# Kernel tuning notes

Hardware: AMD Instinct MI355X
Metric: run time of the kernel (lower is better)

## Reference

```python
import jax, jax.numpy as jnp
import numpy as np

NUM_HEADS = 16


def setup_inputs() -> dict:
    key = jax.random.key(0)
    ks = jax.random.split(key, 8)
    B, W, D = 128, 512, 2048
    s = 1.0 / np.sqrt(D)
    return {
        "x": jax.random.normal(ks[0], (B, D), jnp.float32),
        "buffer": jax.random.normal(ks[1], (B, W, D), jnp.float32),
        "Wq": jax.random.normal(ks[2], (D, D), jnp.float32) * s,
        "Wk": jax.random.normal(ks[3], (D, D), jnp.float32) * s,
        "Wv": jax.random.normal(ks[4], (D, D), jnp.float32) * s,
        "Wo": jax.random.normal(ks[5], (D, D), jnp.float32) * s,
        "Wg": jax.random.normal(ks[6], (D, 2 * D), jnp.float32) * (1.0 / np.sqrt(2 * D)),
        "bg": jnp.zeros((D,), jnp.float32),
    }


def reference(x, buffer, Wq, Wk, Wv, Wo, Wg, bg):
    B, D = x.shape
    H = NUM_HEADS
    Dh = D // H
    scale = Dh ** -0.5
    # steady-state ring buffer update: roll left, append x at last slot
    kv_seq = jnp.concatenate([buffer[:, 1:], x[:, None, :]], axis=1)  # [B, W, D]
    # projections (nn.Linear: y = x @ W.T)
    q = (x @ Wq.T).reshape(B, H, Dh)                      # [B, H, Dh]
    k = (kv_seq @ Wk.T).reshape(B, -1, H, Dh)             # [B, W, H, Dh]
    v = (kv_seq @ Wv.T).reshape(B, -1, H, Dh)
    # single-query attention over the window
    logits = jnp.einsum("bhd,bshd->bhs", q, k) * scale    # [B, H, W]
    attn = jax.nn.softmax(logits, axis=-1)
    out = jnp.einsum("bhs,bshd->bhd", attn, v).reshape(B, D)
    out = out @ Wo.T
    # gated residual
    g = jax.nn.sigmoid(jnp.concatenate([x, out], axis=-1) @ Wg.T + bg)
    return x + g * out
```

## Files before the change

### kernel.cpp

```cpp
#include <hip/hip_runtime.h>
#include <hip/hip_bf16.h>
#include <math.h>

#define B_   128
#define W_   512
#define D_   2048
#define H_   16
#define DH_  128

typedef __attribute__((ext_vector_type(4))) float f32x4;
typedef __attribute__((ext_vector_type(8))) short bf16x8;

typedef const __attribute__((address_space(1))) void* gvp;
typedef __attribute__((address_space(3))) void* lvp;

__device__ inline short f2bf(float f) {
  union { __hip_bfloat16 h; short s; } u;
  u.h = __float2bfloat16(f);
  return u.s;
}
__device__ inline float bf2f(unsigned short u) {
  return __uint_as_float(((unsigned)u) << 16);
}

__device__ inline void pack8_trunc(const float* f, void* dst) {
  unsigned u[4];
#pragma unroll
  for (int j = 0; j < 4; ++j)
    u[j] = __builtin_amdgcn_perm(__float_as_uint(f[2 * j + 1]),
                                 __float_as_uint(f[2 * j]), 0x07060302u);
  *(uint4*)dst = *(const uint4*)u;
}

#define LGKM_BARRIER() do {                                   \
    asm volatile("s_waitcnt lgkmcnt(0)" ::: "memory");        \
    __builtin_amdgcn_sched_barrier(0);                        \
    __builtin_amdgcn_s_barrier();                             \
    __builtin_amdgcn_sched_barrier(0);                        \
  } while (0)

#define VM_LGKM_BARRIER() do {                                \
    asm volatile("s_waitcnt vmcnt(0) lgkmcnt(0)" ::: "memory"); \
    __builtin_amdgcn_sched_barrier(0);                        \
    __builtin_amdgcn_s_barrier();                             \
    __builtin_amdgcn_sched_barrier(0);                        \
  } while (0)

template<bool BBF16, int AMODE, bool TWK>
__global__ __launch_bounds__(256) void gemm_mfma(
    const float* __restrict__ A, int a_rs, long a_hs,
    const float* __restrict__ A2, int a2_k,
    const void* __restrict__ Bv, int b_rs, long b_hs,
    float* __restrict__ C, int c_rs, long c_hs, long c_ks,
    int Kblk,
    const float* __restrict__ twk_src, unsigned short* __restrict__ twk_dst)
{
  __shared__ char sm[2][24576];

  const int t  = threadIdx.x;

  if (TWK) {
    if (blockIdx.x >= 256) {
      float (*tile)[68] = (float(*)[68])sm;
      const int tb  = blockIdx.x - 256;
      const int e0t = (tb & 31) * 64;
      const int d0  = ((tb >> 5) & 1) * 64;
      const int hh  = tb >> 6;
      {
        int d = t >> 2, eq = (t & 3) * 16;
        const float* src = twk_src + (long)(hh * DH_ + d0 + d) * D_ + e0t + eq;
#pragma unroll
        for (int qq = 0; qq < 4; ++qq)
          *(float4*)&tile[d][eq + qq * 4] = *(const float4*)(src + qq * 4);
      }
      __syncthreads();
      {
        int e = t >> 2, dq = (t & 3) * 16;
        unsigned short* dst = twk_dst + ((long)hh * D_ + e0t + e) * DH_ + d0 + dq;
        float f0[8], f1[8];
#pragma unroll
        for (int j = 0; j < 8; ++j) f0[j] = tile[dq + j][e];
#pragma unroll
        for (int j = 0; j < 8; ++j) f1[j] = tile[dq + 8 + j][e];
        pack8_trunc(f0, dst);
        pack8_trunc(f1, dst + 8);
      }
      return;
    }
  }

  const int w  = t >> 6, l = t & 63, lo = l & 15, hi = l >> 4;
  const int wm = w >> 1, wn = w & 1;
  const int n0   = TWK ? ((blockIdx.x & 31) * 64) : (blockIdx.x * 64);
  const int head = TWK ? 0 : blockIdx.y;
  const int ks   = TWK ? ((int)blockIdx.x >> 5) : blockIdx.z;
  const int kbeg = ks * Kblk;
  const int nit  = Kblk >> 6;

  const float* Ab = nullptr;
  if (AMODE == 0) {
    const float* base = A;
    int koff = kbeg;
    if (A2 && kbeg >= a2_k) { base = A2; koff = kbeg - a2_k; }
    Ab = base + head * a_hs + koff;
  }
  const float*          Bf = (const float*)Bv          + (BBF16 ? 0 : head * b_hs + (long)n0 * b_rs + kbeg);
  const unsigned short* Bh = (const unsigned short*)Bv + (BBF16 ? head * b_hs + (long)n0 * b_rs + kbeg : 0);

  const int ar = t >> 2;
  const int ak = (t & 3) * 16;

  f32x4 acc[4][2] = {};

  auto load_tiles = [&](int it, float4* ar4, float4* br4) {
    if (AMODE == 0) {
      const float* Ait = Ab + it * 64;
#pragma unroll
      for (int p = 0; p < 2; ++p) {
        const float* src = Ait + (long)(p * 64 + ar) * a_rs + ak;
#pragma unroll
        for (int qq = 0; qq < 4; ++qq) ar4[p * 4 + qq] = *(const float4*)(src + qq * 4);
      }
    } else {
      const unsigned short* pa = (const unsigned short*)A;
      const float* mlp = A2;
      const int col = kbeg + it * 64 + ak;
#pragma unroll
      for (int p = 0; p < 2; ++p) {
        int m  = p * 64 + ar;
        int bh = m * 16 + head;
        float m0 = mlp[bh * 2],              l0 = mlp[bh * 2 + 1];
        float m1 = mlp[(2048 + bh) * 2],     l1 = mlp[(2048 + bh) * 2 + 1];
        float M  = fmaxf(m0, m1);
        float w0 = __expf(m0 - M), w1 = __expf(m1 - M);
        float inv = 1.0f / (w0 * l0 + w1 * l1);
        w0 *= inv; w1 *= inv;
        const unsigned short* r0 = pa + (long)bh * D_ + col;
        const unsigned short* r1 = r0 + (long)B_ * H_ * D_;
#pragma unroll
        for (int q2 = 0; q2 < 2; ++q2) {
          bf16x8 a0 = *(const bf16x8*)(r0 + q2 * 8);
          bf16x8 a1 = *(const bf16x8*)(r1 + q2 * 8);
          float out[8];
#pragma unroll
          for (int j = 0; j < 8; ++j)
            out[j] = w0 * bf2f((unsigned short)a0[j]) + w1 * bf2f((unsigned short)a1[j]);
          ar4[p * 4 + q2 * 2]     = make_float4(out[0], out[1], out[2], out[3]);
          ar4[p * 4 + q2 * 2 + 1] = make_float4(out[4], out[5], out[6], out[7]);
        }
      }
    }
    if (BBF16) {
      const char* src = (const char*)(Bh + (long)ar * b_rs + it * 64 + ak);
      br4[0] = *(const float4*)(src);
      br4[1] = *(const float4*)(src + 16);
    } else {
      const float* src = Bf + (long)ar * b_rs + it * 64 + ak;
#pragma unroll
      for (int qq = 0; qq < 4; ++qq) br4[qq] = *(const float4*)(src + qq * 4);
    }
  };

  auto write_tiles = [&](int buf, const float4* ar4, const float4* br4) {
    char* As = sm[buf];
    char* Bs = sm[buf] + 16384;
#pragma unroll
    for (int p = 0; p < 2; ++p) {
      int m = p * 64 + ar;
      int base = m * 128 + ak * 2;
      int swz = (m & 7) << 4;
      const float* f = (const float*)(ar4 + p * 4);
#pragma unroll
      for (int h2 = 0; h2 < 2; ++h2)
        pack8_trunc(f + h2 * 8, As + ((base + h2 * 16) ^ swz));
    }
    {
      int n = ar;
      int base = n * 128 + ak * 2;
      int swz = (n & 7) << 4;
      if (BBF16) {
#pragma unroll
        for (int h2 = 0; h2 < 2; ++h2)
          *(bf16x8*)(Bs + ((base + h2 * 16) ^ swz)) = ((const bf16x8*)br4)[h2];
      } else {
        const float* f = (const float*)br4;
#pragma unroll
        for (int h2 = 0; h2 < 2; ++h2)
          pack8_trunc(f + h2 * 8, Bs + ((base + h2 * 16) ^ swz));
      }
    }
  };

  auto compute = [&](int buf) {
    const char* As = sm[buf];
    const char* Bs = sm[buf] + 16384;
#pragma unroll
    for (int kk = 0; kk < 2; ++kk) {
      bf16x8 af[4], bfr[2];
#pragma unroll
      for (int mi = 0; mi < 4; ++mi) {
        int m = wm * 64 + mi * 16 + lo;
        af[mi] = *(const bf16x8*)(As + ((m * 128 + (kk * 32 + hi * 8) * 2) ^ ((m & 7) << 4)));
      }
#pragma unroll
      for (int ni = 0; ni < 2; ++ni) {
        int n = wn * 32 + ni * 16 + lo;
        bfr[ni] = *(const bf16x8*)(Bs + ((n * 128 + (kk * 32 + hi * 8) * 2) ^ ((n & 7) << 4)));
      }
#pragma unroll
      for (int mi = 0; mi < 4; ++mi)
#pragma unroll
        for (int ni = 0; ni < 2; ++ni)
          acc[mi][ni] = __builtin_amdgcn_mfma_f32_16x16x32_bf16(af[mi], bfr[ni], acc[mi][ni], 0, 0, 0);
    }
  };

  float4 ar4[8], br4[4];
  load_tiles(0, ar4, br4);
  write_tiles(0, ar4, br4);
  __syncthreads();
  for (int it = 0; it < nit; ++it) {
    float4 na[8], nb[4];
    if (it + 1 < nit) load_tiles(it + 1, na, nb);
    compute(it & 1);
    if (it + 1 < nit) write_tiles((it + 1) & 1, na, nb);
    __syncthreads();
  }

  float* Cb = C + c_ks * ks + c_hs * head + n0;
#pragma unroll
  for (int mi = 0; mi < 4; ++mi)
#pragma unroll
    for (int ni = 0; ni < 2; ++ni)
#pragma unroll
      for (int r = 0; r < 4; ++r)
        Cb[(long)(wm * 64 + mi * 16 + hi * 4 + r) * c_rs + (wn * 32 + ni * 16 + lo)] = acc[mi][ni][r];
}

__global__ __launch_bounds__(256) void reduce_add_k(
    const float* __restrict__ part, long stride4, float* __restrict__ out)
{
  const long i = (long)blockIdx.x * 256 + threadIdx.x;
  const f32x4* p4 = (const f32x4*)part;
  f32x4 s = p4[i];
#pragma unroll
  for (int k = 1; k < 8; ++k) s += p4[k * stride4 + i];
  ((f32x4*)out)[i] = s;
}

__global__ __launch_bounds__(1024, 4) void fused_attn(
    const float* __restrict__ x, const float* __restrict__ buffer,
    const float* __restrict__ qt, unsigned short* __restrict__ part,
    float* __restrict__ ml)
{
  __shared__ float kv[2 * 8 * 2048];
  __shared__ float lacc[16][9][20];
  __shared__ float pbuf[16][8];
  __shared__ float sbuf[16];

  const int b    = blockIdx.x;
  const int half = blockIdx.y;
  const int t    = threadIdx.x;
  const int w    = t >> 6;
  const int lane = t & 63;
  const int lo   = lane & 15;
  const int hi   = lane >> 4;
  const char* kvb = (const char*)kv;

  bf16x8 afrag[4];
  {
    const float* qrow = qt + ((long)b * H_ + lo) * D_;
    const float sc = 0.088388347648318447f;
#pragma unroll
    for (int kk = 0; kk < 4; ++kk) {
      int e0 = w * 128 + kk * 32 + hi * 8;
      float4 qa = *(const float4*)(qrow + e0);
      float4 qb = *(const float4*)(qrow + e0 + 4);
      afrag[kk][0] = f2bf(qa.x * sc); afrag[kk][1] = f2bf(qa.y * sc);
      afrag[kk][2] = f2bf(qa.z * sc); afrag[kk][3] = f2bf(qa.w * sc);
      afrag[kk][4] = f2bf(qb.x * sc); afrag[kk][5] = f2bf(qb.y * sc);
      afrag[kk][6] = f2bf(qb.z * sc); afrag[kk][7] = f2bf(qb.w * sc);
    }
  }

  float accE[16][2];
#pragma unroll
  for (int h = 0; h < 16; ++h) { accE[h][0] = 0.f; accE[h][1] = 0.f; }
  float m_run = -1e30f, l_run = 0.f;

  auto stage = [&](int sb, int tl) {
#pragma unroll
    for (int r = 0; r < 4; ++r) {
      int s = r * 2 + (w >> 3);
      int inrow = (w & 7) * 1024 + lane * 16;
      int srco = inrow ^ (s << 4);
      int s_glob = half * 256 + tl * 8 + s;
      const float* row = (s_glob < W_ - 1)
          ? buffer + (((long)(b * W_ + s_glob + 1)) << 11)
          : x + ((long)b << 11);
      __builtin_amdgcn_global_load_lds(
          (gvp)(row + (srco >> 2)),
          (lvp)(kv + sb * 16384 + r * 4096 + w * 256), 16, 0, 0);
    }
  };

  stage(0, 0);
  VM_LGKM_BARRIER();
  stage(1, 1);

  for (int tile = 0; tile < 32; ++tile) {
    const int buf  = tile & 1;
    const int bufo = buf * 65536;

    {
      f32x4 c4 = {0.f, 0.f, 0.f, 0.f};
      const int srow = lo & 7;
#pragma unroll
      for (int kk = 0; kk < 4; ++kk) {
        unsigned B0 = (unsigned)(srow * 8192 + (w * 128 + kk * 32 + hi * 8) * 4);
        unsigned o1 = B0 ^ (unsigned)(srow << 4);
        float4 f1 = *(const float4*)(kvb + bufo + o1);
        float4 f2 = *(const float4*)(kvb + bufo + (o1 ^ 16u));
        unsigned u[4];
        u[0] = __builtin_amdgcn_perm(__float_as_uint(f1.y), __float_as_uint(f1.x), 0x07060302u);
        u[1] = __builtin_amdgcn_perm(__float_as_uint(f1.w), __float_as_uint(f1.z), 0x07060302u);
        u[2] = __builtin_amdgcn_perm(__float_as_uint(f2.y), __float_as_uint(f2.x), 0x07060302u);
        u[3] = __builtin_amdgcn_perm(__float_as_uint(f2.w), __float_as_uint(f2.z), 0x07060302u);
        bf16x8 bf;
        __builtin_memcpy(&bf, u, 16);
        c4 = __builtin_amdgcn_mfma_f32_16x16x32_bf16(afrag[kk], bf, c4, 0, 0, 0);
      }
      if (lo < 8) *(f32x4*)&lacc[w][lo][hi * 4] = c4;
    }

    float2 kvp[8];
    {
      const unsigned ebyte = (unsigned)((w * 128 + lane * 2) * 4);
#pragma unroll
      for (int s = 0; s < 8; ++s) {
        unsigned Bx = (unsigned)(s * 8192) + ebyte;
        kvp[s] = *(const float2*)(kvb + bufo + (Bx ^ (unsigned)(s << 4)));
      }
    }
    LGKM_BARRIER();

    if (tile + 2 < 32) stage(buf, tile + 2);

    {
      const int s   = lane & 7;
      const int wwg = lane >> 3;
      float v = lacc[wwg][s][w] + lacc[wwg + 8][s][w];
      v += __shfl_xor(v, 8);
      v += __shfl_xor(v, 16);
      v += __shfl_xor(v, 32);
      float mt = v;
      mt = fmaxf(mt, __shfl_xor(mt, 1));
      mt = fmaxf(mt, __shfl_xor(mt, 2));
      mt = fmaxf(mt, __shfl_xor(mt, 4));
      float m_new = fmaxf(m_run, mt);
      float scl = __expf(m_run - m_new);
      float p = __expf(v - m_new);
      float ps = p;
      ps += __shfl_xor(ps, 1);
      ps += __shfl_xor(ps, 2);
      ps += __shfl_xor(ps, 4);
      l_run = l_run * scl + ps;
      m_run = m_new;
      if (lane < 8) pbuf[w][lane] = p;
      if (lane == 0) sbuf[w] = scl;
    }
    if (tile < 30) {
      asm volatile("s_waitcnt vmcnt(4) lgkmcnt(0)" ::: "memory");
    } else {
      asm volatile("s_waitcnt vmcnt(0) lgkmcnt(0)" ::: "memory");
    }
    __builtin_amdgcn_sched_barrier(0);
    __builtin_amdgcn_s_barrier();
    __builtin_amdgcn_sched_barrier(0);

#pragma unroll
    for (int h = 0; h < 16; ++h) {
      float scl = sbuf[h];
      float a0 = accE[h][0] * scl, a1 = accE[h][1] * scl;
      float4 pA = *(const float4*)&pbuf[h][0];
      float4 pB = *(const float4*)&pbuf[h][4];
      a0 += pA.x * kvp[0].x + pA.y * kvp[1].x + pA.z * kvp[2].x + pA.w * kvp[3].x
          + pB.x * kvp[4].x + pB.y * kvp[5].x + pB.z * kvp[6].x + pB.w * kvp[7].x;
      a1 += pA.x * kvp[0].y + pA.y * kvp[1].y + pA.z * kvp[2].y + pA.w * kvp[3].y
          + pB.x * kvp[4].y + pB.y * kvp[5].y + pB.z * kvp[6].y + pB.w * kvp[7].y;
      accE[h][0] = a0; accE[h][1] = a1;
    }
  }

  {
    long base = ((long)half * B_ + b) * H_;
#pragma unroll
    for (int h = 0; h < 16; ++h) {
      long idx = (base + h) * D_ + w * 128 + lane * 2;
      unsigned u0 = (unsigned short)f2bf(accE[h][0]);
      unsigned u1 = (unsigned short)f2bf(accE[h][1]);
      *(unsigned*)(part + idx) = u0 | (u1 << 16);
    }
    if (lane == 0) {
      ml[(base + w) * 2 + 0] = m_run;
      ml[(base + w) * 2 + 1] = l_run;
    }
  }
}

__global__ __launch_bounds__(256) void gate_final_k(
    const float* __restrict__ part, const float* __restrict__ bg,
    const float* __restrict__ x, const float* __restrict__ out1,
    float* __restrict__ y)
{
  const long i = (long)blockIdx.x * 256 + threadIdx.x;
  const f32x4* p4 = (const f32x4*)part;
  f32x4 z = ((const f32x4*)bg)[i & (D_ / 4 - 1)];
#pragma unroll
  for (int k = 0; k < 8; ++k) z += p4[(long)k * (B_ * D_ / 4) + i];
  f32x4 xv = ((const f32x4*)x)[i];
  f32x4 ov = ((const f32x4*)out1)[i];
  f32x4 r;
#pragma unroll
  for (int j = 0; j < 4; ++j) {
    float g = 1.0f / (1.0f + __expf(-z[j]));
    r[j] = xv[j] + g * ov[j];
  }
  ((f32x4*)y)[i] = r;
}

extern "C" void kernel_launch(void* const* d_in, const int* in_sizes, int n_in,
                              void* d_out, int out_size, void* d_ws, size_t ws_size,
                              hipStream_t stream)
{
  const float* x      = (const float*)d_in[0];
  const float* buffer = (const float*)d_in[1];
  const float* Wq     = (const float*)d_in[2];
  const float* Wk     = (const float*)d_in[3];
  const float* Wv     = (const float*)d_in[4];
  const float* Wo     = (const float*)d_in[5];
  const float* Wg     = (const float*)d_in[6];
  const float* bg     = (const float*)d_in[7];
  float* y = (float*)d_out;

  float* ws    = (float*)d_ws;
  float* q     = ws;
  float* qt    = ws + 262144;
  unsigned short* part_a = (unsigned short*)(ws + 4456448);
  float* ml    = ws + 8650752;
  float* o0    = ws + 8658944;
  float* o1    = ws + 8921088;
  float* partg = ws + 9183232;
  unsigned short* wkT = (unsigned short*)(ws + 11280384);

  const long S = (long)B_ * D_;

  gemm_mfma<false, 0, true><<<dim3(1280), 256, 0, stream>>>(
      x, D_, 0, nullptr, 1 << 30, Wq, D_, 0, partg, D_, 0, S, 256, Wk, wkT);
  reduce_add_k<<<256, 256, 0, stream>>>(partg, S / 4, q);

  gemm_mfma<true, 0, false><<<dim3(32, 16, 1), 256, 0, stream>>>(
      q, D_, DH_, nullptr, 1 << 30, wkT, DH_, (long)D_ * DH_,
      qt, H_ * D_, D_, 0, DH_, nullptr, nullptr);

  fused_attn<<<dim3(B_, 2), 1024, 0, stream>>>(x, buffer, qt, part_a, ml);

  gemm_mfma<false, 1, false><<<dim3(2, 16, 8), 256, 0, stream>>>(
      (const float*)part_a, 0, 0, ml, 0, Wv, D_, (long)DH_ * D_,
      partg, D_, DH_, S, 256, nullptr, nullptr);
  reduce_add_k<<<256, 256, 0, stream>>>(partg, S / 4, o0);

  gemm_mfma<false, 0, false><<<dim3(32, 1, 8), 256, 0, stream>>>(
      o0, D_, 0, nullptr, 1 << 30, Wo, D_, 0, partg, D_, 0, S, 256,
      nullptr, nullptr);
  reduce_add_k<<<256, 256, 0, stream>>>(partg, S / 4, o1);

  gemm_mfma<false, 0, false><<<dim3(32, 1, 8), 256, 0, stream>>>(
      x, D_, 0, o1, D_, Wg, 2 * D_, 0, partg, D_, 0, S, 512,
      nullptr, nullptr);
  gate_final_k<<<256, 256, 0, stream>>>(partg, bg, x, o1, y);

  (void)in_sizes; (void)n_in; (void)out_size; (void)ws_size;
}
```

Baseline: 213.2 us.

## Split gate GEMM and hoist the x-half into the first Q-projection launch

The gate GEMM over concat(x, out) is split in two. The x @ Wg[:, :D] half depends only on x, so it now runs as 128 extra blocks appended to the first launch (Q projection plus Wk transpose), writing 4 K-split partials into a new workspace region. The final gate GEMM then only covers the out half with K=256 splits, and gate_final sums both sets of partials. This takes half the gate GEMM off the serial tail, at the cost of a larger first launch and 4 extra partial reads in the final kernel.

After: 223.3 us. 1.05x slower.

```diff
diff --git a/kernel.cpp b/kernel.cpp
--- a/kernel.cpp
+++ b/kernel.cpp
@@ -53,14 +53,15 @@
     const void* __restrict__ Bv, int b_rs, long b_hs,
     float* __restrict__ C, int c_rs, long c_hs, long c_ks,
     int Kblk,
-    const float* __restrict__ twk_src, unsigned short* __restrict__ twk_dst)
+    const float* __restrict__ twk_src, unsigned short* __restrict__ twk_dst,
+    const float* __restrict__ g6B, float* __restrict__ g6C)
 {
   __shared__ char sm[2][24576];
 
   const int t  = threadIdx.x;
 
   if (TWK) {
-    if (blockIdx.x >= 256) {
+    if (blockIdx.x >= 256 && blockIdx.x < 1280) {
       float (*tile)[68] = (float(*)[68])sm;
       const int tb  = blockIdx.x - 256;
       const int e0t = (tb & 31) * 64;
@@ -89,13 +90,23 @@
     }
   }
 
+  const void* Bv_eff = Bv;
+  float* C_eff = C;
+  int Kblk_eff = Kblk;
+  int brs_eff = b_rs;
+  int bid = blockIdx.x;
+  if (TWK && bid >= 1280) {
+    bid -= 1280;
+    Bv_eff = g6B; C_eff = g6C; Kblk_eff = 512; brs_eff = 2 * D_;
+  }
+
   const int w  = t >> 6, l = t & 63, lo = l & 15, hi = l >> 4;
   const int wm = w >> 1, wn = w & 1;
-  const int n0   = TWK ? ((blockIdx.x & 31) * 64) : (blockIdx.x * 64);
+  const int n0   = TWK ? ((bid & 31) * 64) : (blockIdx.x * 64);
   const int head = TWK ? 0 : blockIdx.y;
-  const int ks   = TWK ? ((int)blockIdx.x >> 5) : blockIdx.z;
-  const int kbeg = ks * Kblk;
-  const int nit  = Kblk >> 6;
+  const int ks   = TWK ? (bid >> 5) : blockIdx.z;
+  const int kbeg = ks * Kblk_eff;
+  const int nit  = Kblk_eff >> 6;
 
   const float* Ab = nullptr;
   if (AMODE == 0) {
@@ -104,8 +115,8 @@
     if (A2 && kbeg >= a2_k) { base = A2; koff = kbeg - a2_k; }
     Ab = base + head * a_hs + koff;
   }
-  const float*          Bf = (const float*)Bv          + (BBF16 ? 0 : head * b_hs + (long)n0 * b_rs + kbeg);
-  const unsigned short* Bh = (const unsigned short*)Bv + (BBF16 ? head * b_hs + (long)n0 * b_rs + kbeg : 0);
+  const float*          Bf = (const float*)Bv_eff      + (BBF16 ? 0 : head * b_hs + (long)n0 * brs_eff + kbeg);
+  const unsigned short* Bh = (const unsigned short*)Bv_eff + (BBF16 ? head * b_hs + (long)n0 * brs_eff + kbeg : 0);
 
   const int ar = t >> 2;
   const int ak = (t & 3) * 16;
@@ -151,11 +162,11 @@
       }
     }
     if (BBF16) {
-      const char* src = (const char*)(Bh + (long)ar * b_rs + it * 64 + ak);
+      const char* src = (const char*)(Bh + (long)ar * brs_eff + it * 64 + ak);
       br4[0] = *(const float4*)(src);
       br4[1] = *(const float4*)(src + 16);
     } else {
-      const float* src = Bf + (long)ar * b_rs + it * 64 + ak;
+      const float* src = Bf + (long)ar * brs_eff + it * 64 + ak;
 #pragma unroll
       for (int qq = 0; qq < 4; ++qq) br4[qq] = *(const float4*)(src + qq * 4);
     }
@@ -227,7 +238,7 @@
     __syncthreads();
   }
 
-  float* Cb = C + c_ks * ks + c_hs * head + n0;
+  float* Cb = C_eff + c_ks * ks + c_hs * head + n0;
 #pragma unroll
   for (int mi = 0; mi < 4; ++mi)
 #pragma unroll
@@ -409,15 +420,18 @@
 }
 
 __global__ __launch_bounds__(256) void gate_final_k(
-    const float* __restrict__ part, const float* __restrict__ bg,
-    const float* __restrict__ x, const float* __restrict__ out1,
-    float* __restrict__ y)
+    const float* __restrict__ p6b, const float* __restrict__ p6a,
+    const float* __restrict__ bg, const float* __restrict__ x,
+    const float* __restrict__ out1, float* __restrict__ y)
 {
   const long i = (long)blockIdx.x * 256 + threadIdx.x;
-  const f32x4* p4 = (const f32x4*)part;
+  const f32x4* pb = (const f32x4*)p6b;
+  const f32x4* pa = (const f32x4*)p6a;
   f32x4 z = ((const f32x4*)bg)[i & (D_ / 4 - 1)];
 #pragma unroll
-  for (int k = 0; k < 8; ++k) z += p4[(long)k * (B_ * D_ / 4) + i];
+  for (int k = 0; k < 8; ++k) z += pb[(long)k * (B_ * D_ / 4) + i];
+#pragma unroll
+  for (int k = 0; k < 4; ++k) z += pa[(long)k * (B_ * D_ / 4) + i];
   f32x4 xv = ((const f32x4*)x)[i];
   f32x4 ov = ((const f32x4*)out1)[i];
   f32x4 r;
@@ -452,33 +466,35 @@
   float* o1    = ws + 8921088;
   float* partg = ws + 9183232;
   unsigned short* wkT = (unsigned short*)(ws + 11280384);
+  float* p6a   = ws + 13377536;
 
   const long S = (long)B_ * D_;
 
-  gemm_mfma<false, 0, true><<<dim3(1280), 256, 0, stream>>>(
-      x, D_, 0, nullptr, 1 << 30, Wq, D_, 0, partg, D_, 0, S, 256, Wk, wkT);
+  gemm_mfma<false, 0, true><<<dim3(1408), 256, 0, stream>>>(
+      x, D_, 0, nullptr, 1 << 30, Wq, D_, 0, partg, D_, 0, S, 256,
+      Wk, wkT, Wg, p6a);
   reduce_add_k<<<256, 256, 0, stream>>>(partg, S / 4, q);
 
   gemm_mfma<true, 0, false><<<dim3(32, 16, 1), 256, 0, stream>>>(
       q, D_, DH_, nullptr, 1 << 30, wkT, DH_, (long)D_ * DH_,
-      qt, H_ * D_, D_, 0, DH_, nullptr, nullptr);
+      qt, H_ * D_, D_, 0, DH_, nullptr, nullptr, nullptr, nullptr);
 
   fused_attn<<<dim3(B_, 2), 1024, 0, stream>>>(x, buffer, qt, part_a, ml);
 
   gemm_mfma<false, 1, false><<<dim3(2, 16, 8), 256, 0, stream>>>(
       (const float*)part_a, 0, 0, ml, 0, Wv, D_, (long)DH_ * D_,
-      partg, D_, DH_, S, 256, nullptr, nullptr);
+      partg, D_, DH_, S, 256, nullptr, nullptr, nullptr, nullptr);
   reduce_add_k<<<256, 256, 0, stream>>>(partg, S / 4, o0);
 
   gemm_mfma<false, 0, false><<<dim3(32, 1, 8), 256, 0, stream>>>(
       o0, D_, 0, nullptr, 1 << 30, Wo, D_, 0, partg, D_, 0, S, 256,
-      nullptr, nullptr);
+      nullptr, nullptr, nullptr, nullptr);
   reduce_add_k<<<256, 256, 0, stream>>>(partg, S / 4, o1);
 
   gemm_mfma<false, 0, false><<<dim3(32, 1, 8), 256, 0, stream>>>(
-      x, D_, 0, o1, D_, Wg, 2 * D_, 0, partg, D_, 0, S, 512,
-      nullptr, nullptr);
-  gate_final_k<<<256, 256, 0, stream>>>(partg, bg, x, o1, y);
+      o1, D_, 0, nullptr, 1 << 30, Wg + D_, 2 * D_, 0, partg, D_, 0, S, 256,
+      nullptr, nullptr, nullptr, nullptr);
+  gate_final_k<<<256, 256, 0, stream>>>(partg, p6a, bg, x, o1, y);
 
   (void)in_sizes; (void)n_in; (void)out_size; (void)ws_size;
 }
```
